# Optimization experiments

Hardware: AMD Instinct MI355X
Metric: run time of the kernel (lower is better)

## Reference

```python
import jax, jax.numpy as jnp
import numpy as np

B, D_MODEL, H, W = 4, 128, 128, 128
HEAD_DIM = 16
GROUP = D_MODEL // HEAD_DIM          # 8 deformable groups
D_INNER = D_MODEL                    # expand = 1
D_STATE = 1
DT_RANK = 8                          # ceil(d_model / 16)
D_CONV = 3
EPS = 1e-6


def setup_inputs() -> dict:
    key = jax.random.key(0)
    ks = jax.random.split(key, 10)
    f = jnp.float32
    # dt bias init as in DASSM.dt_init (dt in [1e-3, 1e-1], inverse-softplus)
    dt = jnp.exp(jax.random.uniform(ks[7], (D_INNER,), f)
                 * (np.log(0.1) - np.log(0.001)) + np.log(0.001))
    dt = jnp.clip(dt, 1e-4)
    dt_b = dt + jnp.log(-jnp.expm1(-dt))
    s = DT_RANK ** -0.5
    return dict(
        x=jax.random.normal(ks[0], (B, D_MODEL, H, W), f),
        in_proj_w=jax.random.normal(ks[1], (D_INNER, D_MODEL), f) * (D_MODEL ** -0.5),
        conv2d_w=jax.random.normal(ks[2], (D_INNER, 1, D_CONV, D_CONV), f) * 0.1,
        conv2d_b=jnp.zeros((D_INNER,), f),
        dw_w=jax.random.normal(ks[3], (D_INNER, 1, 3, 3), f) * 0.1,
        dw_b=jnp.zeros((D_INNER,), f),
        dw_ln_g=jnp.ones((D_INNER,), f),
        dw_ln_b=jnp.zeros((D_INNER,), f),
        off_w=jax.random.normal(ks[4], (GROUP * 2, D_INNER), f) * 0.01,
        off_b=jnp.zeros((GROUP * 2,), f),
        x_proj_w=jax.random.normal(ks[5], (DT_RANK + 2 * D_STATE, D_INNER), f) * (D_INNER ** -0.5),
        dt_w=jax.random.uniform(ks[6], (D_INNER, DT_RANK), f, -s, s),
        dt_b=dt_b,
        A_logs=jnp.tile(jnp.log(jnp.arange(1, D_STATE + 1, dtype=f))[None, :], (D_INNER, 1)),
        Ds=jnp.ones((D_INNER,), f),
        out_ln_g=jnp.ones((D_INNER,), f),
        out_ln_b=jnp.zeros((D_INNER,), f),
        out_proj_w=jax.random.normal(ks[8], (D_MODEL, D_INNER), f) * (D_INNER ** -0.5),
    )


def _layer_norm(x, g, b):
    m = x.mean(-1, keepdims=True)
    v = ((x - m) ** 2).mean(-1, keepdims=True)
    return (x - m) * jax.lax.rsqrt(v + EPS) * g + b


def _dwconv(x, w, b):
    # x: (B,C,H,W), w: (C,1,k,k) depthwise, 'SAME' == torch padding=(k-1)//2
    out = jax.lax.conv_general_dilated(
        x, w, (1, 1), 'SAME', feature_group_count=x.shape[1],
        dimension_numbers=('NCHW', 'OIHW', 'NCHW'))
    return out + b[None, :, None, None]


def _dcn_sample(img_last, offset):
    # DCNv3 with kernel_size=1, mask=1: sampling point = pixel center + offset.
    # img_last: (B,H,W,C); offset: (B,H,W,G*2) laid out (x,y) per group.
    b, h, w, c = img_last.shape
    gc = c // GROUP
    img = img_last.reshape(b, h, w, GROUP, gc)
    off = offset.reshape(b, h, w, GROUP, 2)
    px = jnp.arange(w, dtype=offset.dtype)[None, None, :, None] + off[..., 0]
    py = jnp.arange(h, dtype=offset.dtype)[None, :, None, None] + off[..., 1]
    y0 = jnp.floor(py)
    x0 = jnp.floor(px)
    wy = py - y0
    wx = px - x0
    bi = jnp.arange(b)[:, None, None, None]
    gi = jnp.arange(GROUP)[None, None, None, :]

    def tap(yi, xi, wgt):  # zero-padding bilinear tap (grid_sample, align_corners=False)
        valid = (yi >= 0) & (yi < h) & (xi >= 0) & (xi < w)
        yc = jnp.clip(yi, 0, h - 1).astype(jnp.int32)
        xc = jnp.clip(xi, 0, w - 1).astype(jnp.int32)
        v = img[bi, yc, xc, gi]  # (B,H,W,G,gc)
        return v * (wgt * valid)[..., None]

    out = (tap(y0, x0, (1 - wy) * (1 - wx)) + tap(y0, x0 + 1, (1 - wy) * wx)
           + tap(y0 + 1, x0, wy * (1 - wx)) + tap(y0 + 1, x0 + 1, wy * wx))
    return out.reshape(b, h, w, c)


def _selective_scan(xs, dts, A, Bs, Cs, Ds, dt_bias):
    # xs,dts: (B,D,L); A: (D,N); Bs,Cs: (B,N,L); delta_softplus=True
    delta = jax.nn.softplus(dts + dt_bias[None, :, None])
    dA = jnp.exp(jnp.einsum('bdl,dn->lbdn', delta, A))          # (L,B,D,N)
    dBx = jnp.einsum('bdl,bnl,bdl->lbdn', delta, Bs, xs)          # (L,B,D,N)
    C_t = jnp.transpose(Cs, (2, 0, 1))                            # (L,B,N)

    def step(hc, inputs):
        dA_t, dBx_t, c = inputs
        hc = dA_t * hc + dBx_t
        return hc, jnp.einsum('bdn,bn->bd', hc, c)

    h0 = jnp.zeros(dA.shape[1:], xs.dtype)
    _, ys = jax.lax.scan(step, h0, (dA, dBx, C_t))                # ys: (L,B,D)
    y = jnp.transpose(ys, (1, 2, 0))                              # (B,D,L)
    return y + Ds[None, :, None] * xs


def reference(x, in_proj_w, conv2d_w, conv2d_b, dw_w, dw_b, dw_ln_g, dw_ln_b,
              off_w, off_b, x_proj_w, dt_w, dt_b, A_logs, Ds,
              out_ln_g, out_ln_b, out_proj_w):
    # in_proj (1x1 conv, no bias) then depthwise conv + SiLU
    xin = jnp.einsum('bchw,oc->bohw', x, in_proj_w)
    xc = jax.nn.silu(_dwconv(xin, conv2d_w, conv2d_b))
    # Dynamic_Adaptive_Scan: dwconv -> LN(channels_last) -> GELU -> offsets -> DCNv3(k=1)
    x1 = _dwconv(xc, dw_w, dw_b)
    x1 = jax.nn.gelu(_layer_norm(jnp.transpose(x1, (0, 2, 3, 1)), dw_ln_g, dw_ln_b),
                     approximate=False)
    offset = x1 @ off_w.T + off_b                                  # (B,H,W,G*2)
    xd = _dcn_sample(jnp.transpose(xc, (0, 2, 3, 1)), offset)      # (B,H,W,C)
    xd = jnp.transpose(xd, (0, 3, 1, 2))                           # (B,C,H,W)
    # SSM (Mamba selective scan over L = H*W)
    Bn, C, Hh, Ww = xd.shape
    L = Hh * Ww
    xs = xd.reshape(Bn, C, L)
    x_dbl = jnp.einsum('rc,bcl->brl', x_proj_w, xs)
    dts, Bs, Cs = jnp.split(x_dbl, [DT_RANK, DT_RANK + D_STATE], axis=1)
    dts = jnp.einsum('dr,brl->bdl', dt_w, dts)
    A = -jnp.exp(A_logs)
    y = _selective_scan(xs, dts, A, Bs, Cs, Ds, dt_b).reshape(Bn, C, Hh, Ww)
    # out LayerNorm (over channels) + out_proj (1x1, no bias)
    y = jnp.transpose(_layer_norm(jnp.transpose(y, (0, 2, 3, 1)), out_ln_g, out_ln_b),
                      (0, 3, 1, 2))
    return jnp.einsum('bchw,oc->bohw', y, out_proj_w)
```

## Files before the change

### kernel.cpp

```cpp
#include <hip/hip_runtime.h>
#include <hip/hip_bf16.h>

typedef unsigned short u16;
typedef unsigned int u32;
typedef __bf16 bf16x8 __attribute__((ext_vector_type(8)));
typedef float f32x4 __attribute__((ext_vector_type(4)));

__device__ __forceinline__ float bfu(u16 u) { return __uint_as_float(((u32)u) << 16); }
__device__ __forceinline__ u16 fbf(float f) {
  __hip_bfloat16 h = __float2bfloat16(f);
  return *reinterpret_cast<u16*>(&h);
}
__device__ __forceinline__ float softplusf(float z) {
  float t = __expf(z);
  return (z > 20.f) ? z : __logf(1.f + t);
}
__device__ __forceinline__ float lo16(u32 p) { return __uint_as_float(p << 16); }
__device__ __forceinline__ float hi16(u32 p) { return __uint_as_float(p & 0xffff0000u); }
__device__ __forceinline__ bf16x8 ld_bf8(const u16* p) {
  union { uint4 u; bf16x8 v; } c;
  c.u = *(const uint4*)p;
  return c.v;
}

__global__ __launch_bounds__(256) void k_inproj(const float* __restrict__ X,
                                                const float* __restrict__ W,
                                                u16* __restrict__ out,
                                                const float* __restrict__ W2,
                                                const float* __restrict__ gO,
                                                const float* __restrict__ bO,
                                                float* __restrict__ s12) {
  __shared__ __align__(16) u16 Ws[128 * 136];
  __shared__ __align__(16) u16 Xs[64 * 136];
  int tid = threadIdx.x;
  if (blockIdx.x == 1024) {
    if (tid < 128) {
      int o = tid;
      float s1 = 0.f, s2 = 0.f;
      for (int c = 0; c < 128; ++c) {
        float w = W2[(o << 7) + c];
        s1 = fmaf(w, bO[c], s1);
        s2 = fmaf(w, gO[c], s2);
      }
      s12[o] = s1;
      s12[128 + o] = s2;
    }
    return;
  }
  int b = blockIdx.x >> 8;
  int l0 = (blockIdx.x & 255) << 6;
  for (int i = 0; i < 16; ++i) {
    int idx = (i << 8) + tid;
    int o = idx >> 5, c4 = (idx & 31) << 2;
    float4 w4 = *(const float4*)&W[(o << 7) + c4];
    ushort4 s;
    s.x = fbf(w4.x); s.y = fbf(w4.y); s.z = fbf(w4.z); s.w = fbf(w4.w);
    *(ushort4*)&Ws[o * 136 + c4] = s;
  }
  for (int i = 0; i < 8; ++i) {
    int idx = (i << 8) + tid;
    int c = idx >> 4, lq = (idx & 15) << 2;
    float4 x4 = *(const float4*)&X[(((long)(b << 7) + c) << 14) + l0 + lq];
    Xs[(lq + 0) * 136 + c] = fbf(x4.x);
    Xs[(lq + 1) * 136 + c] = fbf(x4.y);
    Xs[(lq + 2) * 136 + c] = fbf(x4.z);
    Xs[(lq + 3) * 136 + c] = fbf(x4.w);
  }
  __syncthreads();
  int w = tid >> 6, lane = tid & 63;
  int mrow = lane & 15, quad = lane >> 4;
  f32x4 acc[2][4];
#pragma unroll
  for (int ot = 0; ot < 2; ++ot)
#pragma unroll
    for (int lt = 0; lt < 4; ++lt) acc[ot][lt] = (f32x4){0.f, 0.f, 0.f, 0.f};
#pragma unroll
  for (int kb = 0; kb < 4; ++kb) {
    int c0 = (kb << 5) + (quad << 3);
    bf16x8 af[2], bfr[4];
#pragma unroll
    for (int ot = 0; ot < 2; ++ot)
      af[ot] = ld_bf8(&Ws[((w << 5) + (ot << 4) + mrow) * 136 + c0]);
#pragma unroll
    for (int lt = 0; lt < 4; ++lt)
      bfr[lt] = ld_bf8(&Xs[((lt << 4) + mrow) * 136 + c0]);
#pragma unroll
    for (int ot = 0; ot < 2; ++ot)
#pragma unroll
      for (int lt = 0; lt < 4; ++lt)
        acc[ot][lt] = __builtin_amdgcn_mfma_f32_16x16x32_bf16(af[ot], bfr[lt], acc[ot][lt], 0, 0, 0);
  }
#pragma unroll
  for (int ot = 0; ot < 2; ++ot)
#pragma unroll
    for (int lt = 0; lt < 4; ++lt) {
      int l = l0 + (lt << 4) + mrow;
      int o = (w << 5) + (ot << 4) + (quad << 2);
      ushort4 s;
      s.x = fbf(acc[ot][lt][0]); s.y = fbf(acc[ot][lt][1]);
      s.z = fbf(acc[ot][lt][2]); s.w = fbf(acc[ot][lt][3]);
      *(ushort4*)&out[(((long)(b << 14) + l) << 7) + o] = s;
    }
}

__global__ __launch_bounds__(256) void k_dwconv(const u16* __restrict__ in,
                                                const float* __restrict__ w9,
                                                const float* __restrict__ bias,
                                                u16* __restrict__ out) {
  __shared__ float wsT[9][128];
  __shared__ float bs[128];
  int tid = threadIdx.x;
  for (int i = 0; i < 5; ++i) {
    int lin = (i << 8) + tid;
    if (lin < 1152) { int c = lin / 9, k = lin - 9 * c; wsT[k][c] = w9[lin]; }
  }
  if (tid < 128) bs[tid] = bias[tid];
  __syncthreads();
  int blk = blockIdx.x;
  int b = blk >> 10;
  int s = blk & 1023;
  int h = s >> 3;
  int w = ((s & 7) << 4) + (tid >> 4);
  int c0 = (tid & 15) << 3;
  const u16* bbase = in + ((long)b << 21);
  float acc[8];
  {
    float4 b0 = *(const float4*)&bs[c0];
    float4 b1 = *(const float4*)&bs[c0 + 4];
    acc[0] = b0.x; acc[1] = b0.y; acc[2] = b0.z; acc[3] = b0.w;
    acc[4] = b1.x; acc[5] = b1.y; acc[6] = b1.z; acc[7] = b1.w;
  }
#pragma unroll
  for (int ky = -1; ky <= 1; ++ky) {
    int y = h + ky;
    if ((unsigned)y >= 128u) continue;
#pragma unroll
    for (int kx = -1; kx <= 1; ++kx) {
      int x = w + kx;
      if ((unsigned)x >= 128u) continue;
      int k = (ky + 1) * 3 + (kx + 1);
      uint4 v = *(const uint4*)(bbase + ((((y << 7) + x)) << 7) + c0);
      float4 w0 = *(const float4*)&wsT[k][c0];
      float4 w1 = *(const float4*)&wsT[k][c0 + 4];
      u32 vv[4] = {v.x, v.y, v.z, v.w};
      float wf[8] = {w0.x, w0.y, w0.z, w0.w, w1.x, w1.y, w1.z, w1.w};
#pragma unroll
      for (int cc = 0; cc < 8; ++cc) {
        float xv = (cc & 1) ? hi16(vv[cc >> 1]) : lo16(vv[cc >> 1]);
        acc[cc] = fmaf(wf[cc], xv, acc[cc]);
      }
    }
  }
#pragma unroll
  for (int cc = 0; cc < 8; ++cc) acc[cc] = acc[cc] / (1.f + __expf(-acc[cc]));
  ushort4 s0, s1;
  s0.x = fbf(acc[0]); s0.y = fbf(acc[1]); s0.z = fbf(acc[2]); s0.w = fbf(acc[3]);
  s1.x = fbf(acc[4]); s1.y = fbf(acc[5]); s1.z = fbf(acc[6]); s1.w = fbf(acc[7]);
  u16* po = out + ((long)b << 21) + ((((h << 7) + w)) << 7) + c0;
  *(ushort4*)po = s0;
  *(ushort4*)(po + 4) = s1;
}

__global__ __launch_bounds__(256) void k_dwoff(const u16* __restrict__ in,
                                               const float* __restrict__ w9,
                                               const float* __restrict__ bias,
                                               const float* __restrict__ g,
                                               const float* __restrict__ bt,
                                               const float* __restrict__ offw,
                                               const float* __restrict__ offb,
                                               float* __restrict__ offs) {
  __shared__ float wsT[9][128];
  __shared__ float bs[128], gs[128], bsh[128];
  __shared__ __align__(16) u16 Ge[16 * 136];
  __shared__ __align__(16) u16 Wos[16 * 136];
  int tid = threadIdx.x;
  for (int i = 0; i < 5; ++i) {
    int lin = (i << 8) + tid;
    if (lin < 1152) { int c = lin / 9, k = lin - 9 * c; wsT[k][c] = w9[lin]; }
  }
  if (tid < 128) { bs[tid] = bias[tid]; gs[tid] = g[tid]; bsh[tid] = bt[tid]; }
  for (int i = 0; i < 8; ++i) {
    int idx = (i << 8) + tid;
    int o = idx >> 7, c = idx & 127;
    Wos[o * 136 + c] = fbf(offw[idx]);
  }
  __syncthreads();
  int blk = blockIdx.x;
  int b = blk >> 10;
  int s = blk & 1023;
  int h = s >> 3;
  int p = tid >> 4;
  int w = ((s & 7) << 4) + p;
  int c0 = (tid & 15) << 3;
  const u16* bbase = in + ((long)b << 21);
  float acc[8];
  {
    float4 b0 = *(const float4*)&bs[c0];
    float4 b1 = *(const float4*)&bs[c0 + 4];
    acc[0] = b0.x; acc[1] = b0.y; acc[2] = b0.z; acc[3] = b0.w;
    acc[4] = b1.x; acc[5] = b1.y; acc[6] = b1.z; acc[7] = b1.w;
  }
#pragma unroll
  for (int ky = -1; ky <= 1; ++ky) {
    int y = h + ky;
    if ((unsigned)y >= 128u) continue;
#pragma unroll
    for (int kx = -1; kx <= 1; ++kx) {
      int x = w + kx;
      if ((unsigned)x >= 128u) continue;
      int k = (ky + 1) * 3 + (kx + 1);
      uint4 v = *(const uint4*)(bbase + ((((y << 7) + x)) << 7) + c0);
      float4 w0 = *(const float4*)&wsT[k][c0];
      float4 w1 = *(const float4*)&wsT[k][c0 + 4];
      u32 vv[4] = {v.x, v.y, v.z, v.w};
      float wf[8] = {w0.x, w0.y, w0.z, w0.w, w1.x, w1.y, w1.z, w1.w};
#pragma unroll
      for (int cc = 0; cc < 8; ++cc) {
        float xv = (cc & 1) ? hi16(vv[cc >> 1]) : lo16(vv[cc >> 1]);
        acc[cc] = fmaf(wf[cc], xv, acc[cc]);
      }
    }
  }
  float sum = 0.f, ssum = 0.f;
#pragma unroll
  for (int cc = 0; cc < 8; ++cc) { sum += acc[cc]; ssum = fmaf(acc[cc], acc[cc], ssum); }
#pragma unroll
  for (int off = 1; off < 16; off <<= 1) {
    sum += __shfl_xor(sum, off);
    ssum += __shfl_xor(ssum, off);
  }
  float m = sum * (1.f / 128.f);
  float r = rsqrtf(ssum * (1.f / 128.f) - m * m + 1e-6f);
  {
    u32 pk[4];
#pragma unroll
    for (int jj = 0; jj < 4; ++jj) {
      u16 h2[2];
#pragma unroll
      for (int e = 0; e < 2; ++e) {
        int cc = 2 * jj + e;
        float xn = fmaf((acc[cc] - m) * r, gs[c0 + cc], bsh[c0 + cc]);
        h2[e] = fbf(0.5f * xn * (1.f + erff(xn * 0.70710678118f)));
      }
      pk[jj] = (u32)h2[0] | ((u32)h2[1] << 16);
    }
    *(uint4*)&Ge[p * 136 + c0] = make_uint4(pk[0], pk[1], pk[2], pk[3]);
  }
  __syncthreads();
  if (tid < 64) {
    int lane = tid;
    int mrow = lane & 15, quad = lane >> 4;
    f32x4 acc0 = (f32x4){0.f, 0.f, 0.f, 0.f};
#pragma unroll
    for (int kb = 0; kb < 4; ++kb) {
      int cb = (kb << 5) + (quad << 3);
      bf16x8 af = ld_bf8(&Wos[mrow * 136 + cb]);
      bf16x8 bfr = ld_bf8(&Ge[mrow * 136 + cb]);
      acc0 = __builtin_amdgcn_mfma_f32_16x16x32_bf16(af, bfr, acc0, 0, 0, 0);
    }
    int l = (h << 7) + ((s & 7) << 4) + mrow;
    float2* po = (float2*)offs;
    int o0 = quad << 2;
    po[(((long)((b << 3) + (quad << 1))) << 14) + l] =
        make_float2(acc0[0] + offb[o0], acc0[1] + offb[o0 + 1]);
    po[(((long)((b << 3) + (quad << 1) + 1)) << 14) + l] =
        make_float2(acc0[2] + offb[o0 + 2], acc0[3] + offb[o0 + 3]);
  }
}

__global__ __launch_bounds__(512, 8) void k_dcn(const u16* __restrict__ xc,
                                                const float* __restrict__ offs,
                                                const float* __restrict__ xpw,
                                                const float* __restrict__ dtw,
                                                u16* __restrict__ xs,
                                                u16* __restrict__ dts,
                                                float* __restrict__ Bsb,
                                                float* __restrict__ Csb) {
  __shared__ __align__(16) u16 xds_bf[64 * 132];
  __shared__ float part[64 * 81];
  __shared__ __align__(16) float xdblT[8 * 64];
  int tid = threadIdx.x;
  int blk = blockIdx.x;
  int b = blk >> 8;
  int l0 = (blk & 255) << 6;
  int p = tid & 63, gg = tid >> 6;
  int l = l0 + p, hh = l >> 7, ww = l & 127;
  float2 off = ((const float2*)offs)[(((long)((b << 3) + gg)) << 14) + l];
  float px = (float)ww + off.x, py = (float)hh + off.y;
  float x0f = floorf(px), y0f = floorf(py);
  float wx = px - x0f, wy = py - y0f;
  int ix = (int)x0f, iy = (int)y0f;
  int x0c = min(max(ix, 0), 127), x1c = min(max(ix + 1, 0), 127);
  int y0c = min(max(iy, 0), 127), y1c = min(max(iy + 1, 0), 127);
  float vx0 = ((unsigned)ix < 128u) ? 1.f : 0.f;
  float vx1 = ((unsigned)(ix + 1) < 128u) ? 1.f : 0.f;
  float vy0 = ((unsigned)iy < 128u) ? 1.f : 0.f;
  float vy1 = ((unsigned)(iy + 1) < 128u) ? 1.f : 0.f;
  float wt4[4] = {(1.f - wy) * (1.f - wx) * vy0 * vx0,
                  (1.f - wy) * wx * vy0 * vx1,
                  wy * (1.f - wx) * vy1 * vx0,
                  wy * wx * vy1 * vx1};
  const u16* bbase = xc + ((long)b << 21) + (gg << 4);
  const u16* tp[4];
  tp[0] = bbase + ((((y0c << 7) + x0c)) << 7);
  tp[1] = bbase + ((((y0c << 7) + x1c)) << 7);
  tp[2] = bbase + ((((y1c << 7) + x0c)) << 7);
  tp[3] = bbase + ((((y1c << 7) + x1c)) << 7);
  float acc[16];
#pragma unroll
  for (int ch = 0; ch < 16; ++ch) acc[ch] = 0.f;
#pragma unroll
  for (int t = 0; t < 4; ++t) {
    uint4 v0 = *(const uint4*)tp[t];
    uint4 v1 = *(const uint4*)(tp[t] + 8);
    float wv = wt4[t];
    u32 vv[8] = {v0.x, v0.y, v0.z, v0.w, v1.x, v1.y, v1.z, v1.w};
#pragma unroll
    for (int ch = 0; ch < 16; ++ch) {
      float xv = (ch & 1) ? hi16(vv[ch >> 1]) : lo16(vv[ch >> 1]);
      acc[ch] = fmaf(wv, xv, acc[ch]);
    }
  }
  {
    u32 pk[8];
#pragma unroll
    for (int j = 0; j < 8; ++j)
      pk[j] = (u32)fbf(acc[2 * j]) | ((u32)fbf(acc[2 * j + 1]) << 16);
    u16* row = &xds_bf[p * 132 + (gg << 4)];
#pragma unroll
    for (int q = 0; q < 4; ++q)
      *(uint2*)(row + (q << 2)) = make_uint2(pk[2 * q], pk[2 * q + 1]);
  }
  {
    int ggu = __builtin_amdgcn_readfirstlane(gg);
    const float* wb = xpw + (ggu << 4);
    int pbase = p * 81 + gg;
#pragma unroll
    for (int r = 0; r < 10; ++r) {
      const float* wr = wb + (r << 7);
      float s = 0.f;
#pragma unroll
      for (int ch = 0; ch < 16; ++ch) s = fmaf(wr[ch], acc[ch], s);
      part[pbase + (r << 3)] = s;
    }
  }
  __syncthreads();
  {
    int task = tid;
#pragma unroll
    for (int pass = 0; pass < 2; ++pass, task += 512) {
      if (task < 640) {
        int r = task >> 6, p2 = task & 63;
        const float* pp = &part[p2 * 81 + (r << 3)];
        float s = ((pp[0] + pp[1]) + (pp[2] + pp[3])) + ((pp[4] + pp[5]) + (pp[6] + pp[7]));
        if (r < 8) xdblT[(r << 6) + p2] = s;
        else if (r == 8) Bsb[((long)b << 14) + l0 + p2] = s;
        else Csb[((long)b << 14) + l0 + p2] = s;
      }
    }
  }
#pragma unroll
  for (int it = 0; it < 2; ++it) {
    int task = (it << 9) + tid;
    int cc = task >> 3, t = task & 7;
    u32 pk[4];
#pragma unroll
    for (int jj = 0; jj < 4; ++jj) {
      u16 a0 = xds_bf[((t << 3) + 2 * jj + 0) * 132 + cc];
      u16 a1 = xds_bf[((t << 3) + 2 * jj + 1) * 132 + cc];
      pk[jj] = (u32)a0 | ((u32)a1 << 16);
    }
    *(uint4*)&xs[(((long)(b << 7) + cc) << 14) + l0 + (t << 3)] =
        make_uint4(pk[0], pk[1], pk[2], pk[3]);
  }
  __syncthreads();
  {
    int dd = tid >> 3, t = tid & 7;
    float4 a0 = *(const float4*)&dtw[dd << 3];
    float4 a1 = *(const float4*)&dtw[(dd << 3) + 4];
    float4 b0 = *(const float4*)&dtw[(dd + 64) << 3];
    float4 b1 = *(const float4*)&dtw[((dd + 64) << 3) + 4];
    float wr0[8] = {a0.x, a0.y, a0.z, a0.w, a1.x, a1.y, a1.z, a1.w};
    float wr1[8] = {b0.x, b0.y, b0.z, b0.w, b1.x, b1.y, b1.z, b1.w};
    float y0[8], y1[8];
#pragma unroll
    for (int j = 0; j < 8; ++j) { y0[j] = 0.f; y1[j] = 0.f; }
#pragma unroll
    for (int rr = 0; rr < 8; ++rr) {
      float w0 = wr0[rr], w1 = wr1[rr];
      const float* xr = &xdblT[(rr << 6) + (t << 3)];
      float4 xa = *(const float4*)xr;
      float4 xb = *(const float4*)(xr + 4);
      float xv[8] = {xa.x, xa.y, xa.z, xa.w, xb.x, xb.y, xb.z, xb.w};
#pragma unroll
      for (int j = 0; j < 8; ++j) {
        y0[j] = fmaf(w0, xv[j], y0[j]);
        y1[j] = fmaf(w1, xv[j], y1[j]);
      }
    }
    u32 pk0[4], pk1[4];
#pragma unroll
    for (int jj = 0; jj < 4; ++jj) {
      pk0[jj] = (u32)fbf(y0[2 * jj]) | ((u32)fbf(y0[2 * jj + 1]) << 16);
      pk1[jj] = (u32)fbf(y1[2 * jj]) | ((u32)fbf(y1[2 * jj + 1]) << 16);
    }
    *(uint4*)&dts[(((long)(b << 7) + dd) << 14) + l0 + (t << 3)] =
        make_uint4(pk0[0], pk0[1], pk0[2], pk0[3]);
    *(uint4*)&dts[(((long)(b << 7) + dd + 64) << 14) + l0 + (t << 3)] =
        make_uint4(pk1[0], pk1[1], pk1[2], pk1[3]);
  }
}

__global__ __launch_bounds__(1024) void k_scan(u16* __restrict__ xy,
                                               const u16* __restrict__ dts16,
                                               const float* __restrict__ Bsb,
                                               const float* __restrict__ Csb,
                                               const float* __restrict__ A_logs,
                                               const float* __restrict__ Dsv,
                                               const float* __restrict__ dtbv) {
  __shared__ float swp[16], swe[16];
  int bd = blockIdx.x;
  int b = bd >> 7, d = bd & 127;
  float Ad = -__expf(A_logs[d]);
  float dtb = dtbv[d];
  float Dd = Dsv[d];
  int t = threadIdx.x;
  int lane = t & 63, wid = t >> 6;
  long base = ((long)bd << 14) + (t << 4);
  long bb = ((long)b << 14) + (t << 4);
  const uint4* pz4 = (const uint4*)(dts16 + base);
  const uint4* px4 = (const uint4*)(xy + base);
  const float4* pB = (const float4*)(Bsb + bb);
  const float4* pC = (const float4*)(Csb + bb);
  uint4 zA = pz4[0], zB = pz4[1];
  uint4 xA = px4[0], xB = px4[1];
  u32 zw[8] = {zA.x, zA.y, zA.z, zA.w, zB.x, zB.y, zB.z, zB.w};
  u32 xw[8] = {xA.x, xA.y, xA.z, xA.w, xB.x, xB.y, xB.z, xB.w};
  float E = 0.f, P = 1.f;
#pragma unroll
  for (int q = 0; q < 4; ++q) {
    float4 B4 = pB[q];
    float Bq[4] = {B4.x, B4.y, B4.z, B4.w};
#pragma unroll
    for (int j = 0; j < 4; ++j) {
      int k = (q << 2) + j;
      float z = (k & 1) ? hi16(zw[k >> 1]) : lo16(zw[k >> 1]);
      float xv = (k & 1) ? hi16(xw[k >> 1]) : lo16(xw[k >> 1]);
      float delta = softplusf(z + dtb);
      float a = __expf(delta * Ad);
      E = fmaf(a, E, delta * Bq[j] * xv);
      P *= a;
    }
  }
#pragma unroll
  for (int off = 1; off < 64; off <<= 1) {
    float Pp = __shfl_up(P, off);
    float Ep = __shfl_up(E, off);
    if (lane >= off) { E = fmaf(P, Ep, E); P *= Pp; }
  }
  if (lane == 63) { swp[wid] = P; swe[wid] = E; }
  __syncthreads();
  if (t < 16) {
    float p2 = swp[t], e2 = swe[t];
#pragma unroll
    for (int off = 1; off < 16; off <<= 1) {
      float pp = __shfl_up(p2, off);
      float ee = __shfl_up(e2, off);
      if (t >= off) { e2 = fmaf(p2, ee, e2); p2 *= pp; }
    }
    swp[t] = p2; swe[t] = e2;
  }
  __syncthreads();
  float hw = (wid == 0) ? 0.f : swe[wid - 1];
  float Pex = __shfl_up(P, 1);
  float Eex = __shfl_up(E, 1);
  if (lane == 0) { Pex = 1.f; Eex = 0.f; }
  float h = fmaf(Pex, hw, Eex);
  u32 ypk[8];
#pragma unroll
  for (int q = 0; q < 4; ++q) {
    float4 B4 = pB[q];
    float4 C4 = pC[q];
    float Bq[4] = {B4.x, B4.y, B4.z, B4.w};
    float Cq[4] = {C4.x, C4.y, C4.z, C4.w};
#pragma unroll
    for (int j = 0; j < 4; ++j) {
      int k = (q << 2) + j;
      float z = (k & 1) ? hi16(zw[k >> 1]) : lo16(zw[k >> 1]);
      float xv = (k & 1) ? hi16(xw[k >> 1]) : lo16(xw[k >> 1]);
      float delta = softplusf(z + dtb);
      float a = __expf(delta * Ad);
      h = fmaf(a, h, delta * Bq[j] * xv);
      u16 yb = fbf(fmaf(Dd, xv, h * Cq[j]));
      if ((k & 1) == 0) ypk[k >> 1] = yb; else ypk[k >> 1] |= (u32)yb << 16;
    }
  }
  uint4* py = (uint4*)(xy + base);
  py[0] = make_uint4(ypk[0], ypk[1], ypk[2], ypk[3]);
  py[1] = make_uint4(ypk[4], ypk[5], ypk[6], ypk[7]);
}

__global__ __launch_bounds__(256) void k_outproj(const u16* __restrict__ y,
                                                 const float* __restrict__ W2,
                                                 const float* __restrict__ g,
                                                 const float* __restrict__ s12,
                                                 float* __restrict__ out) {
  __shared__ __align__(16) u16 Ws[128 * 136];
  __shared__ __align__(16) u16 Ys[64 * 136];
  __shared__ float ps[4][64], pss[4][64];
  __shared__ float mean_s[64], rstd_s[64];
  int tid = threadIdx.x;
  int b = blockIdx.x >> 8;
  int l0 = (blockIdx.x & 255) << 6;
  for (int i = 0; i < 16; ++i) {
    int idx = (i << 8) + tid;
    int o = idx >> 5, c4 = (idx & 31) << 2;
    float4 w4 = *(const float4*)&W2[(o << 7) + c4];
    ushort4 s;
    s.x = fbf(w4.x * g[c4]);     s.y = fbf(w4.y * g[c4 + 1]);
    s.z = fbf(w4.z * g[c4 + 2]); s.w = fbf(w4.w * g[c4 + 3]);
    *(ushort4*)&Ws[o * 136 + c4] = s;
  }
  for (int i = 0; i < 4; ++i) {
    int idx = (i << 8) + tid;
    int c = idx >> 3, lq = (idx & 7) << 3;
    uint4 v = *(const uint4*)&y[(((long)(b << 7) + c) << 14) + l0 + lq];
    u32 vv[4] = {v.x, v.y, v.z, v.w};
#pragma unroll
    for (int r = 0; r < 8; ++r)
      Ys[(lq + r) * 136 + c] = (u16)((r & 1) ? (vv[r >> 1] >> 16) : (vv[r >> 1] & 0xffffu));
  }
  __syncthreads();
  {
    int l = tid & 63, q = tid >> 6;
    const u16* row = &Ys[l * 136 + (q << 5)];
    float s = 0.f, ss = 0.f;
#pragma unroll 8
    for (int c = 0; c < 32; ++c) { float v = bfu(row[c]); s += v; ss = fmaf(v, v, ss); }
    ps[q][l] = s; pss[q][l] = ss;
  }
  __syncthreads();
  if (tid < 64) {
    float s = ps[0][tid] + ps[1][tid] + ps[2][tid] + ps[3][tid];
    float ss = pss[0][tid] + pss[1][tid] + pss[2][tid] + pss[3][tid];
    float m = s * (1.f / 128.f);
    mean_s[tid] = m;
    rstd_s[tid] = rsqrtf(ss * (1.f / 128.f) - m * m + 1e-6f);
  }
  __syncthreads();
  int w = tid >> 6, lane = tid & 63;
  int mrow = lane & 15, quad = lane >> 4;
  f32x4 acc[2][4];
#pragma unroll
  for (int ot = 0; ot < 2; ++ot)
#pragma unroll
    for (int lt = 0; lt < 4; ++lt) acc[ot][lt] = (f32x4){0.f, 0.f, 0.f, 0.f};
#pragma unroll
  for (int kb = 0; kb < 4; ++kb) {
    int c0 = (kb << 5) + (quad << 3);
    bf16x8 af[2], bfr[4];
#pragma unroll
    for (int ot = 0; ot < 2; ++ot)
      af[ot] = ld_bf8(&Ws[((w << 5) + (ot << 4) + mrow) * 136 + c0]);
#pragma unroll
    for (int lt = 0; lt < 4; ++lt)
      bfr[lt] = ld_bf8(&Ys[((lt << 4) + mrow) * 136 + c0]);
#pragma unroll
    for (int ot = 0; ot < 2; ++ot)
#pragma unroll
      for (int lt = 0; lt < 4; ++lt)
        acc[ot][lt] = __builtin_amdgcn_mfma_f32_16x16x32_bf16(af[ot], bfr[lt], acc[ot][lt], 0, 0, 0);
  }
  float s1r[2][4], s2r[2][4];
#pragma unroll
  for (int ot = 0; ot < 2; ++ot)
#pragma unroll
    for (int r = 0; r < 4; ++r) {
      int o = (w << 5) + (ot << 4) + (quad << 2) + r;
      s1r[ot][r] = s12[o];
      s2r[ot][r] = s12[128 + o];
    }
#pragma unroll
  for (int ot = 0; ot < 2; ++ot)
#pragma unroll
    for (int lt = 0; lt < 4; ++lt) {
      int lcol = (lt << 4) + mrow;
      float mv = mean_s[lcol], rv = rstd_s[lcol];
      int obase = (w << 5) + (ot << 4) + (quad << 2);
#pragma unroll
      for (int r = 0; r < 4; ++r) {
        float v = fmaf(rv, acc[ot][lt][r] - mv * s2r[ot][r], s1r[ot][r]);
        out[(((long)(b << 7) + obase + r) << 14) + l0 + lcol] = v;
      }
    }
}

extern "C" void kernel_launch(void* const* d_in, const int* in_sizes, int n_in,
                              void* d_out, int out_size, void* d_ws, size_t ws_size,
                              hipStream_t stream) {
  const float* x         = (const float*)d_in[0];
  const float* in_proj_w = (const float*)d_in[1];
  const float* conv2d_w  = (const float*)d_in[2];
  const float* conv2d_b  = (const float*)d_in[3];
  const float* dw_w      = (const float*)d_in[4];
  const float* dw_b      = (const float*)d_in[5];
  const float* dw_ln_g   = (const float*)d_in[6];
  const float* dw_ln_b   = (const float*)d_in[7];
  const float* off_w     = (const float*)d_in[8];
  const float* off_b     = (const float*)d_in[9];
  const float* x_proj_w  = (const float*)d_in[10];
  const float* dt_w      = (const float*)d_in[11];
  const float* dt_b      = (const float*)d_in[12];
  const float* A_logs    = (const float*)d_in[13];
  const float* Ds        = (const float*)d_in[14];
  const float* out_ln_g  = (const float*)d_in[15];
  const float* out_ln_b  = (const float*)d_in[16];
  const float* out_proj_w= (const float*)d_in[17];
  float* out = (float*)d_out;

  u16* A  = (u16*)d_ws;
  u16* Bx = A + 8388608;
  u16* Dd = Bx + 8388608;
  float* offs  = (float*)(Dd + 8388608);
  float* Bsb   = offs + 1048576;
  float* Csb   = Bsb + 65536;
  float* s12   = Csb + 65536;

  hipLaunchKernelGGL(k_inproj, dim3(1025), dim3(256), 0, stream, x, in_proj_w, A,
                     out_proj_w, out_ln_g, out_ln_b, s12);
  hipLaunchKernelGGL(k_dwconv, dim3(4096), dim3(256), 0, stream, A, conv2d_w, conv2d_b, Bx);
  hipLaunchKernelGGL(k_dwoff, dim3(4096), dim3(256), 0, stream, Bx, dw_w, dw_b,
                     dw_ln_g, dw_ln_b, off_w, off_b, offs);
  hipLaunchKernelGGL(k_dcn, dim3(1024), dim3(512), 0, stream, Bx, offs, x_proj_w, dt_w, A, Dd, Bsb, Csb);
  hipLaunchKernelGGL(k_scan, dim3(512), dim3(1024), 0, stream, A, Dd, Bsb, Csb, A_logs, Ds, dt_b);
  hipLaunchKernelGGL(k_outproj, dim3(1024), dim3(256), 0, stream, A, out_proj_w, out_ln_g, s12, out);
}
```

Baseline: 221.5 us.

## Store conv output group-major so deformable sampling reads contiguous 64-byte pairs

The silu-conv output is now written in a group-major layout (B, 8 groups, H*W, 16 channels) instead of channels-last with 128-channel pixels. The depthwise-offset kernel and the DCN sampler read through this new layout. Horizontally adjacent bilinear taps become contiguous 64-byte runs, so each row loads with four 16-byte vector loads. Edge clamping is handled by selecting the duplicated pixel, which relies on the x0c+1 read staying inside the buffer even when clamped.

```diff
diff --git a/kernel.cpp b/kernel.cpp
--- a/kernel.cpp
+++ b/kernel.cpp
@@ -22,6 +22,7 @@
   c.u = *(const uint4*)p;
   return c.v;
 }
+
 
 __global__ __launch_bounds__(256) void k_inproj(const float* __restrict__ X,
                                                 const float* __restrict__ W,
@@ -153,12 +154,14 @@
   }
 #pragma unroll
   for (int cc = 0; cc < 8; ++cc) acc[cc] = acc[cc] / (1.f + __expf(-acc[cc]));
-  ushort4 s0, s1;
-  s0.x = fbf(acc[0]); s0.y = fbf(acc[1]); s0.z = fbf(acc[2]); s0.w = fbf(acc[3]);
-  s1.x = fbf(acc[4]); s1.y = fbf(acc[5]); s1.z = fbf(acc[6]); s1.w = fbf(acc[7]);
-  u16* po = out + ((long)b << 21) + ((((h << 7) + w)) << 7) + c0;
-  *(ushort4*)po = s0;
-  *(ushort4*)(po + 4) = s1;
+  int g4 = c0 >> 4, sub = c0 & 15;
+  uint4 pkst;
+  pkst.x = (u32)fbf(acc[0]) | ((u32)fbf(acc[1]) << 16);
+  pkst.y = (u32)fbf(acc[2]) | ((u32)fbf(acc[3]) << 16);
+  pkst.z = (u32)fbf(acc[4]) | ((u32)fbf(acc[5]) << 16);
+  pkst.w = (u32)fbf(acc[6]) | ((u32)fbf(acc[7]) << 16);
+  u16* po = out + (((long)(b << 3) + g4) << 18) + ((((h << 7) + w)) << 4) + sub;
+  *(uint4*)po = pkst;
 }
 
 __global__ __launch_bounds__(256) void k_dwoff(const u16* __restrict__ in,
@@ -192,7 +195,8 @@
   int p = tid >> 4;
   int w = ((s & 7) << 4) + p;
   int c0 = (tid & 15) << 3;
-  const u16* bbase = in + ((long)b << 21);
+  int g4 = c0 >> 4, sub = c0 & 15;
+  const u16* bbase = in + (((long)(b << 3) + g4) << 18) + sub;
   float acc[8];
   {
     float4 b0 = *(const float4*)&bs[c0];
@@ -209,7 +213,7 @@
       int x = w + kx;
       if ((unsigned)x >= 128u) continue;
       int k = (ky + 1) * 3 + (kx + 1);
-      uint4 v = *(const uint4*)(bbase + ((((y << 7) + x)) << 7) + c0);
+      uint4 v = *(const uint4*)(bbase + ((((y << 7) + x)) << 4));
       float4 w0 = *(const float4*)&wsT[k][c0];
       float4 w1 = *(const float4*)&wsT[k][c0 + 4];
       u32 vv[4] = {v.x, v.y, v.z, v.w};
@@ -300,26 +304,36 @@
                   (1.f - wy) * wx * vy0 * vx1,
                   wy * (1.f - wx) * vy1 * vx0,
                   wy * wx * vy1 * vx1};
-  const u16* bbase = xc + ((long)b << 21) + (gg << 4);
-  const u16* tp[4];
-  tp[0] = bbase + ((((y0c << 7) + x0c)) << 7);
-  tp[1] = bbase + ((((y0c << 7) + x1c)) << 7);
-  tp[2] = bbase + ((((y1c << 7) + x0c)) << 7);
-  tp[3] = bbase + ((((y1c << 7) + x1c)) << 7);
+  const u16* bbase = xc + (((long)(b << 3) + gg) << 18);
+  const u16* r0p = bbase + ((((y0c << 7) + x0c)) << 4);
+  const u16* r1p = bbase + ((((y1c << 7) + x0c)) << 4);
+  uint4 q0 = ((const uint4*)r0p)[0];
+  uint4 q1 = ((const uint4*)r0p)[1];
+  uint4 q2 = ((const uint4*)r0p)[2];
+  uint4 q3 = ((const uint4*)r0p)[3];
+  uint4 q4 = ((const uint4*)r1p)[0];
+  uint4 q5 = ((const uint4*)r1p)[1];
+  uint4 q6 = ((const uint4*)r1p)[2];
+  uint4 q7 = ((const uint4*)r1p)[3];
+  bool adj = (x1c != x0c);
+  u32 t0[8] = {q0.x, q0.y, q0.z, q0.w, q1.x, q1.y, q1.z, q1.w};
+  u32 t1[8] = {adj ? q2.x : q0.x, adj ? q2.y : q0.y, adj ? q2.z : q0.z, adj ? q2.w : q0.w,
+               adj ? q3.x : q1.x, adj ? q3.y : q1.y, adj ? q3.z : q1.z, adj ? q3.w : q1.w};
+  u32 t2[8] = {q4.x, q4.y, q4.z, q4.w, q5.x, q5.y, q5.z, q5.w};
+  u32 t3[8] = {adj ? q6.x : q4.x, adj ? q6.y : q4.y, adj ? q6.z : q4.z, adj ? q6.w : q4.w,
+               adj ? q7.x : q5.x, adj ? q7.y : q5.y, adj ? q7.z : q5.z, adj ? q7.w : q5.w};
   float acc[16];
 #pragma unroll
   for (int ch = 0; ch < 16; ++ch) acc[ch] = 0.f;
 #pragma unroll
-  for (int t = 0; t < 4; ++t) {
-    uint4 v0 = *(const uint4*)tp[t];
-    uint4 v1 = *(const uint4*)(tp[t] + 8);
-    float wv = wt4[t];
-    u32 vv[8] = {v0.x, v0.y, v0.z, v0.w, v1.x, v1.y, v1.z, v1.w};
-#pragma unroll
-    for (int ch = 0; ch < 16; ++ch) {
-      float xv = (ch & 1) ? hi16(vv[ch >> 1]) : lo16(vv[ch >> 1]);
-      acc[ch] = fmaf(wv, xv, acc[ch]);
-    }
+  for (int ch = 0; ch < 16; ++ch) {
+    float v0 = (ch & 1) ? hi16(t0[ch >> 1]) : lo16(t0[ch >> 1]);
+    float v1 = (ch & 1) ? hi16(t1[ch >> 1]) : lo16(t1[ch >> 1]);
+    float v2 = (ch & 1) ? hi16(t2[ch >> 1]) : lo16(t2[ch >> 1]);
+    float v3 = (ch & 1) ? hi16(t3[ch >> 1]) : lo16(t3[ch >> 1]);
+    float a = fmaf(wt4[0], v0, wt4[1] * v1);
+    a = fmaf(wt4[2], v2, a);
+    acc[ch] = fmaf(wt4[3], v3, a);
   }
   {
     u32 pk[8];
```

Measured after the change: 218.8 us. Within noise of the previous version (-1.2%).
